# Kernel optimization log

Measured on AMD Instinct MI355X. Metric: run time of the kernel, lower is better.

## Reference

```python
import jax, jax.numpy as jnp
import numpy as np

N, S, C, P, K = 64, 64, 128, 32, 1000   # batch, frames, in_planes, part_num, class_num
HPG = (3 * C) // 16                      # hidden channels per group for part_score mlp = 24
EPS = 1e-5


def setup_inputs() -> dict:
    key = jax.random.key(0)
    ks = jax.random.split(key, 8)
    return {
        "t_f": jax.random.normal(ks[0], (N, S, C, P), jnp.float32),
        "t_s": jax.random.normal(ks[1], (N, S, C, P), jnp.float32),
        "t_l": jax.random.normal(ks[2], (N, S, C, P), jnp.float32),
        # part_score grouped 1x1 convs (groups=P): per-group (out, in)
        "w1": jax.random.normal(ks[3], (P, HPG, 3 * C), jnp.float32) * 0.05,
        "bn1_gamma": jnp.ones((P, HPG), jnp.float32),
        "bn1_beta": jnp.zeros((P, HPG), jnp.float32),
        "w2": jax.random.normal(ks[4], (P, 1, HPG), jnp.float32) * 0.05,
        # decay_channel grouped 1x1 conv: per-group 3C -> C
        "wd": jax.random.normal(ks[5], (P, C, 3 * C), jnp.float32) * 0.05,
        # per-part BatchNorm1d(C) affine params
        "bn_gamma": jnp.ones((P, C), jnp.float32),
        "bn_beta": jnp.zeros((P, C), jnp.float32),
        # fc: (1, C, K) in torch; squeeze leading 1
        "fc": jax.random.normal(ks[6], (C, K), jnp.float32) * 0.05,
    }


def reference(t_f, t_s, t_l, w1, bn1_gamma, bn1_beta, w2, wd, bn_gamma, bn_beta, fc):
    # cat along channel dim then arrange as (n, p, 3c, s) == grouped conv layout
    x = jnp.concatenate([t_f, t_s, t_l], axis=2).transpose(0, 3, 2, 1)  # (n,p,3c,s)

    # --- part_score: grouped 1x1 conv -> BN (batch stats over n,s) -> LeakyReLU -> grouped conv -> sigmoid
    h = jnp.einsum('npis,poi->npos', x, w1)               # (n,p,HPG,s)
    mu = h.mean(axis=(0, 3), keepdims=True)
    var = h.var(axis=(0, 3), keepdims=True)               # biased var (torch training BN)
    h = (h - mu) / jnp.sqrt(var + EPS) * bn1_gamma[None, :, :, None] + bn1_beta[None, :, :, None]
    h = jnp.where(h >= 0, h, 0.01 * h)                    # LeakyReLU(0.01)
    score = jax.nn.sigmoid(jnp.einsum('npis,poi->npos', h, w2))  # (n,p,1,s)

    # --- decay_channel grouped 1x1 conv: 3c -> c per part
    feat = jnp.einsum('npis,poi->npos', x, wd)            # (n,p,c,s)

    # attention-weighted temporal pooling
    wpv = (feat * score).sum(-1) / score.sum(-1)          # (n,p,c)

    # per-part BatchNorm1d over batch dim (training-mode batch stats)
    m = wpv.mean(axis=0)                                  # (p,c)
    v = wpv.var(axis=0)
    part_feature = ((wpv - m) / jnp.sqrt(v + EPS) * bn_gamma + bn_beta).transpose(1, 0, 2)  # (p,n,c)

    part_classification = jnp.einsum('pnc,ck->pnk', part_feature, fc)  # (p,n,K)

    # argmax frame per (n,p) and gather from t_f
    idx = jnp.argmax(score[:, :, 0, :], axis=-1)          # (n,p)
    tfp = t_f.transpose(0, 3, 1, 2)                       # (n,p,s,c)
    selected = jnp.take_along_axis(tfp, idx[:, :, None, None], axis=2)[:, :, 0, :]  # (n,p,c)
    selected_part_feature = selected.transpose(1, 0, 2)   # (p,n,c)

    weighted_part_vector = wpv.transpose(1, 0, 2)         # (p,n,c)
    return part_classification, weighted_part_vector, selected_part_feature
```

## Files before the change

### kernel.cpp

```cpp
#include <hip/hip_runtime.h>
#include <math.h>

#define N 64
#define S 64
#define C 128
#define P 32
#define KCLS 1000
#define HPG 24
#define C3 384
#define NS 4096
#define EPSV 1e-5f

#define WS_H    0
#define WS_W1Z  (WS_H + 2*P*HPG*NS)
#define WS_BNSS (WS_W1Z + 384*8*32*4)
#define WS_Y    (WS_BNSS + P*HPG*2)
#define WS_Z    (WS_Y + P*N*C3)
#define WS_PF   (WS_Z + P*N)
#define WS_SC   (WS_PF + P*C*N)
#define WS_MI   (WS_SC + N*P*S)

__global__ __launch_bounds__(256) void k0w_w1z(
    const float* __restrict__ w1, float* __restrict__ w1z)
{
  int e = blockIdx.x * 256 + threadIdx.x;
  int p = e & 31;
  int r = e >> 5;
  int j = r % 3;
  int r2 = r / 3;
  int og = r2 & 3;
  int i = r2 >> 2;
  float2 v;
  v.x = w1[(p * HPG + og * 6 + j * 2 + 0) * C3 + i];
  v.y = w1[(p * HPG + og * 6 + j * 2 + 1) * C3 + i];
  ((float2*)w1z)[e] = v;
}

__global__ __launch_bounds__(256) void k01_h(
    const float* __restrict__ tf, const float* __restrict__ ts,
    const float* __restrict__ tl, const float* __restrict__ w1z,
    float* __restrict__ h)
{
  int n = blockIdx.x, st = blockIdx.y, split = blockIdx.z;
  int s0 = st * 8;
  int t = threadIdx.x;
  int p = t & 31;
  int og = (t >> 5) & 3;
  int sh = t >> 7;
  __shared__ float xl[8192];
  float acc[6][4];
  #pragma unroll
  for (int oo = 0; oo < 6; ++oo)
    #pragma unroll
    for (int s = 0; s < 4; ++s) acc[oo][s] = 0.f;

  const float2* w2p = (const float2*)w1z;
  const float* srcs[3] = {tf, ts, tl};
  const float* xp = &xl[sh * 4096 + p];

  for (int ch = 0; ch < 6; ++ch) {
    int gch = split * 6 + ch;
    int z = gch >> 2, c0 = (gch & 3) * 32;
    const float* base = srcs[z] + ((size_t)(n * S + s0)) * C * P + c0 * P;
    if (ch) __syncthreads();
    #pragma unroll
    for (int j = 0; j < 8; ++j) {
      int e = t + 256 * j;
      int s_loc = e >> 8;
      int idx = e & 255;
      float4 v = *(const float4*)&base[(size_t)s_loc * C * P + idx * 4];
      *(float4*)&xl[s_loc * 1024 + idx * 4] = v;
    }
    __syncthreads();
    #pragma unroll 4
    for (int cl = 0; cl < 32; ++cl) {
      int i = gch * 32 + cl;
      float xs[4];
      #pragma unroll
      for (int ss = 0; ss < 4; ++ss)
        xs[ss] = xp[ss * 1024 + cl * 32];
      int wb = ((i * 4 + og) * 3) * 32 + p;
      float2 wa  = w2p[wb];
      float2 wbv = w2p[wb + 32];
      float2 wc  = w2p[wb + 64];
      #pragma unroll
      for (int ss = 0; ss < 4; ++ss) {
        acc[0][ss] += wa.x  * xs[ss];
        acc[1][ss] += wa.y  * xs[ss];
        acc[2][ss] += wbv.x * xs[ss];
        acc[3][ss] += wbv.y * xs[ss];
        acc[4][ss] += wc.x  * xs[ss];
        acc[5][ss] += wc.y  * xs[ss];
      }
    }
  }
  #pragma unroll
  for (int oo = 0; oo < 6; ++oo) {
    int o = og * 6 + oo;
    float* hp = h + ((size_t)split * P * HPG + p * HPG + o) * NS + n * S + s0 + sh * 4;
    *(float4*)hp = make_float4(acc[oo][0], acc[oo][1], acc[oo][2], acc[oo][3]);
  }
}

__global__ __launch_bounds__(256) void k2_bnstat(const float* __restrict__ h,
    const float* __restrict__ g, const float* __restrict__ b,
    float* __restrict__ bnss)
{
  int po = blockIdx.x;
  int t = threadIdx.x;
  const float4* r0 = (const float4*)(h + (size_t)po * NS);
  const float4* r1 = (const float4*)(h + (size_t)(P * HPG + po) * NS);
  float sm = 0.f, sq = 0.f;
  #pragma unroll
  for (int k = 0; k < 4; ++k) {
    float4 a = r0[t + 256 * k];
    float4 c = r1[t + 256 * k];
    float v0 = a.x + c.x, v1 = a.y + c.y, v2 = a.z + c.z, v3 = a.w + c.w;
    sm += v0 + v1 + v2 + v3;
    sq += v0 * v0 + v1 * v1 + v2 * v2 + v3 * v3;
  }
  #pragma unroll
  for (int m = 1; m < 64; m <<= 1) {
    sm += __shfl_xor(sm, m, 64);
    sq += __shfl_xor(sq, m, 64);
  }
  __shared__ float red[4][2];
  int w = t >> 6;
  if ((t & 63) == 0) { red[w][0] = sm; red[w][1] = sq; }
  __syncthreads();
  if (t == 0) {
    float sum = red[0][0] + red[1][0] + red[2][0] + red[3][0];
    float ssq = red[0][1] + red[1][1] + red[2][1] + red[3][1];
    float mu  = sum / (float)NS;
    float var = ssq / (float)NS - mu * mu;
    float sc = g[po] * rsqrtf(var + EPSV);
    bnss[po * 2]     = sc;
    bnss[po * 2 + 1] = b[po] - mu * sc;
  }
}

__global__ __launch_bounds__(256) void k3a_score(
    const float* __restrict__ h, const float* __restrict__ bnss,
    const float* __restrict__ w2,
    float* __restrict__ score, float* __restrict__ z,
    int* __restrict__ mi_out)
{
  int n = blockIdx.x;
  int p = blockIdx.y * 4 + (threadIdx.x >> 6);
  int l = threadIdx.x & 63;
  float ssum = 0.f;
  const float* hp0 = h + (size_t)p * HPG * NS + n * S;
  const float* hp1 = hp0 + (size_t)P * HPG * NS;
  #pragma unroll
  for (int o = 0; o < HPG; ++o) {
    float hv = hp0[(size_t)o * NS + l] + hp1[(size_t)o * NS + l];
    float sc = bnss[(p * HPG + o) * 2];
    float sh = bnss[(p * HPG + o) * 2 + 1];
    float v = hv * sc + sh;
    v = (v >= 0.f) ? v : 0.01f * v;
    ssum += w2[p * HPG + o] * v;
  }
  float scr = 1.f / (1.f + expf(-ssum));
  float zs = scr;
  #pragma unroll
  for (int m = 1; m < 64; m <<= 1) zs += __shfl_xor(zs, m, 64);
  float mv = scr; int mi = l;
  #pragma unroll
  for (int m = 1; m < 64; m <<= 1) {
    float ov = __shfl_xor(mv, m, 64);
    int   oi = __shfl_xor(mi, m, 64);
    if (ov > mv || (ov == mv && oi < mi)) { mv = ov; mi = oi; }
  }
  if (l == 0) { z[p * N + n] = zs; mi_out[n * P + p] = mi; }
  score[((size_t)n * P + p) * S + l] = scr;
}

__global__ __launch_bounds__(256) void k3b_y(
    const float* __restrict__ tf, const float* __restrict__ ts,
    const float* __restrict__ tl, const float* __restrict__ score,
    const int* __restrict__ mi, float* __restrict__ y,
    float* __restrict__ out_spf)
{
  int n = blockIdx.x, chunk = blockIdx.y;
  int z = chunk >> 2, c0 = (chunk & 3) * 32;
  const float* src = (z == 0) ? tf : (z == 1) ? ts : tl;
  int t = threadIdx.x;
  int p = t & 31, cl = t >> 5;
  __shared__ float sc_lds[S * P];
  __shared__ int mi_lds[P];
  #pragma unroll
  for (int j = 0; j < 8; ++j) {
    int e = t + 256 * j;
    int s2 = e >> 5, pp = e & 31;
    sc_lds[s2 * P + pp] = score[((size_t)n * P + pp) * S + s2];
  }
  if (t < P) mi_lds[t] = mi[n * P + t];
  __syncthreads();
  int mymi = mi_lds[p];
  const float* base = src + (size_t)n * S * C * P + (size_t)(c0 + cl) * P + p;
  float acc[4] = {0.f, 0.f, 0.f, 0.f};
  float sel[4] = {0.f, 0.f, 0.f, 0.f};
  #pragma unroll 8
  for (int s = 0; s < S; ++s) {
    float scv = sc_lds[s * P + p];
    #pragma unroll
    for (int j = 0; j < 4; ++j) {
      float v = base[(size_t)s * C * P + j * 8 * P];
      acc[j] += v * scv;
      sel[j] = (s == mymi) ? v : sel[j];
    }
  }
  float* yp = y + ((size_t)p * N + n) * C3 + z * C + c0 + cl;
  #pragma unroll
  for (int j = 0; j < 4; ++j) yp[j * 8] = acc[j];
  if (z == 0) {
    float* sp = out_spf + ((size_t)p * N + n) * C + c0 + cl;
    #pragma unroll
    for (int j = 0; j < 4; ++j) sp[j * 8] = sel[j];
  }
}

__global__ __launch_bounds__(256) void k4_wpv(
    const float* __restrict__ y, const float* __restrict__ z,
    const float* __restrict__ wd, const float* __restrict__ g,
    const float* __restrict__ b, float* __restrict__ out_wpv,
    float* __restrict__ pf)
{
  int p   = blockIdx.x;
  int cch = blockIdx.y;
  int t = threadIdx.x;
  int n = t & 63, cg = t >> 6;
  int cbase = cch * 16 + cg * 4;
  __shared__ float ych[96][66];
  float acc[4] = {0.f, 0.f, 0.f, 0.f};
  const float* yp  = y  + (size_t)p * N * C3;
  const float* wdp = wd + (size_t)p * C * C3;
  for (int ch = 0; ch < 4; ++ch) {
    __syncthreads();
    #pragma unroll
    for (int j = 0; j < 24; ++j) {
      int e = t + 256 * j;
      int i = e % 96, nn = e / 96;
      ych[i][nn] = yp[nn * C3 + ch * 96 + i];
    }
    __syncthreads();
    #pragma unroll
    for (int sub = 0; sub < 4; ++sub) {
      float yr[24];
      #pragma unroll
      for (int kk = 0; kk < 24; ++kk) yr[kk] = ych[sub * 24 + kk][n];
      int ibase = ch * 96 + sub * 24;
      #pragma unroll
      for (int cl = 0; cl < 4; ++cl) {
        const float4* w4 = (const float4*)(wdp + (size_t)(cbase + cl) * C3 + ibase);
        float a = 0.f;
        #pragma unroll
        for (int q = 0; q < 6; ++q) {
          float4 wv = w4[q];
          a += yr[q*4+0] * wv.x + yr[q*4+1] * wv.y
             + yr[q*4+2] * wv.z + yr[q*4+3] * wv.w;
        }
        acc[cl] += a;
      }
    }
  }
  float zinv = 1.f / z[p * N + n];
  #pragma unroll
  for (int cl = 0; cl < 4; ++cl) acc[cl] *= zinv;
  #pragma unroll
  for (int cl = 0; cl < 4; ++cl) {
    float v = acc[cl];
    float s = v, q = v * v;
    #pragma unroll
    for (int m = 1; m < 64; m <<= 1) {
      s += __shfl_xor(s, m, 64);
      q += __shfl_xor(q, m, 64);
    }
    float mu  = s * (1.f / 64.f);
    float var = q * (1.f / 64.f) - mu * mu;
    int c = cbase + cl;
    float sc = g[p * C + c] * rsqrtf(var + EPSV);
    float sh = b[p * C + c] - mu * sc;
    pf[((size_t)p * C + c) * N + n] = v * sc + sh;
  }
  float4 wout = make_float4(acc[0], acc[1], acc[2], acc[3]);
  *(float4*)(out_wpv + ((size_t)p * N + n) * C + cbase) = wout;
}

__global__ __launch_bounds__(256) void k5_fc(
    const float* __restrict__ pf, const float* __restrict__ fc,
    float* __restrict__ out0)
{
  int kt = blockIdx.x;
  int p  = blockIdx.y;
  int n0 = blockIdx.z * 16;
  int t = threadIdx.x;
  int k = kt * 256 + t;
  bool ok = k < KCLS;
  int kk = ok ? k : (KCLS - 1);
  float acc[16];
  #pragma unroll
  for (int j = 0; j < 16; ++j) acc[j] = 0.f;
  for (int c = 0; c < C; ++c) {
    float fv = fc[c * KCLS + kk];
    const float4* row4 = (const float4*)(pf + ((size_t)p * C + c) * N + n0);
    #pragma unroll
    for (int j4 = 0; j4 < 4; ++j4) {
      float4 r = row4[j4];
      acc[j4*4+0] += r.x * fv; acc[j4*4+1] += r.y * fv;
      acc[j4*4+2] += r.z * fv; acc[j4*4+3] += r.w * fv;
    }
  }
  if (ok) {
    #pragma unroll 4
    for (int j = 0; j < 16; ++j)
      out0[(size_t)(p * N + n0 + j) * KCLS + k] = acc[j];
  }
}

extern "C" void kernel_launch(void* const* d_in, const int* in_sizes, int n_in,
                              void* d_out, int out_size, void* d_ws, size_t ws_size,
                              hipStream_t stream)
{
  const float* tf = (const float*)d_in[0];
  const float* ts = (const float*)d_in[1];
  const float* tl = (const float*)d_in[2];
  const float* w1 = (const float*)d_in[3];
  const float* g1 = (const float*)d_in[4];
  const float* b1 = (const float*)d_in[5];
  const float* w2 = (const float*)d_in[6];
  const float* wd = (const float*)d_in[7];
  const float* g  = (const float*)d_in[8];
  const float* b  = (const float*)d_in[9];
  const float* fc = (const float*)d_in[10];

  float* ws   = (float*)d_ws;
  float* h    = ws + WS_H;
  float* w1z  = ws + WS_W1Z;
  float* bnss = ws + WS_BNSS;
  float* y    = ws + WS_Y;
  float* z    = ws + WS_Z;
  float* pf   = ws + WS_PF;
  float* sc   = ws + WS_SC;
  int*   mi   = (int*)(ws + WS_MI);

  float* out0 = (float*)d_out;
  float* out1 = out0 + P * N * KCLS;
  float* out2 = out1 + P * N * C;

  k0w_w1z<<<576, 256, 0, stream>>>(w1, w1z);
  k01_h<<<dim3(64, 8, 2), 256, 0, stream>>>(tf, ts, tl, w1z, h);
  k2_bnstat<<<768, 256, 0, stream>>>(h, g1, b1, bnss);
  k3a_score<<<dim3(64, 8), 256, 0, stream>>>(h, bnss, w2, sc, z, mi);
  k3b_y<<<dim3(64, 12), 256, 0, stream>>>(tf, ts, tl, sc, mi, y, out2);
  k4_wpv<<<dim3(32, 8), 256, 0, stream>>>(y, z, wd, g, b, out1, pf);
  k5_fc<<<dim3(4, 32, 4), 256, 0, stream>>>(pf, fc, out0);
}
```

Baseline: 197.1 us.

## Split input-channel reduction across thread halves with 8-frame register tiles in h kernel

```diff
diff --git a/kernel.cpp b/kernel.cpp
--- a/kernel.cpp
+++ b/kernel.cpp
@@ -12,8 +12,8 @@
 #define EPSV 1e-5f
 
 #define WS_H    0
-#define WS_W1Z  (WS_H + 2*P*HPG*NS)
-#define WS_BNSS (WS_W1Z + 384*8*32*4)
+#define WS_W1Z  (WS_H + 4*P*HPG*NS)
+#define WS_BNSS (WS_W1Z + 384*4*3*32*2)
 #define WS_Y    (WS_BNSS + P*HPG*2)
 #define WS_Z    (WS_Y + P*N*C3)
 #define WS_PF   (WS_Z + P*N)
@@ -28,11 +28,11 @@
   int r = e >> 5;
   int j = r % 3;
   int r2 = r / 3;
-  int og = r2 & 3;
+  int oq = r2 & 3;
   int i = r2 >> 2;
   float2 v;
-  v.x = w1[(p * HPG + og * 6 + j * 2 + 0) * C3 + i];
-  v.y = w1[(p * HPG + og * 6 + j * 2 + 1) * C3 + i];
+  v.x = w1[(p * HPG + oq * 6 + j * 2 + 0) * C3 + i];
+  v.y = w1[(p * HPG + oq * 6 + j * 2 + 1) * C3 + i];
   ((float2*)w1z)[e] = v;
 }
 
@@ -45,46 +45,51 @@
   int s0 = st * 8;
   int t = threadIdx.x;
   int p = t & 31;
-  int og = (t >> 5) & 3;
-  int sh = t >> 7;
+  int oq = (t >> 5) & 3;
+  int ih = t >> 7;
   __shared__ float xl[8192];
-  float acc[6][4];
+  float acc[6][8];
   #pragma unroll
   for (int oo = 0; oo < 6; ++oo)
     #pragma unroll
-    for (int s = 0; s < 4; ++s) acc[oo][s] = 0.f;
+    for (int s = 0; s < 8; ++s) acc[oo][s] = 0.f;
 
   const float2* w2p = (const float2*)w1z;
   const float* srcs[3] = {tf, ts, tl};
-  const float* xp = &xl[sh * 4096 + p];
 
   for (int ch = 0; ch < 6; ++ch) {
     int gch = split * 6 + ch;
     int z = gch >> 2, c0 = (gch & 3) * 32;
-    const float* base = srcs[z] + ((size_t)(n * S + s0)) * C * P + c0 * P;
+    const float* tb = srcs[z] + ((size_t)(n * S + s0)) * C * P + c0 * P;
     if (ch) __syncthreads();
     #pragma unroll
     for (int j = 0; j < 8; ++j) {
-      int e = t + 256 * j;
-      int s_loc = e >> 8;
-      int idx = e & 255;
-      float4 v = *(const float4*)&base[(size_t)s_loc * C * P + idx * 4];
-      *(float4*)&xl[s_loc * 1024 + idx * 4] = v;
+      int a = (t + 256 * j) * 4;
+      int c  = a >> 8;
+      int sh = (a >> 7) & 1;
+      int pp = (a >> 2) & 31;
+      const float* g = tb + (size_t)(sh * 4) * C * P + c * P + pp;
+      float4 v;
+      v.x = g[0];
+      v.y = g[(size_t)1 * C * P];
+      v.z = g[(size_t)2 * C * P];
+      v.w = g[(size_t)3 * C * P];
+      *(float4*)&xl[a] = v;
     }
     __syncthreads();
     #pragma unroll 4
-    for (int cl = 0; cl < 32; ++cl) {
+    for (int k = 0; k < 16; ++k) {
+      int cl = ih * 16 + k;
       int i = gch * 32 + cl;
-      float xs[4];
-      #pragma unroll
-      for (int ss = 0; ss < 4; ++ss)
-        xs[ss] = xp[ss * 1024 + cl * 32];
-      int wb = ((i * 4 + og) * 3) * 32 + p;
+      int wb = ((i * 4 + oq) * 3) * 32 + p;
       float2 wa  = w2p[wb];
       float2 wbv = w2p[wb + 32];
       float2 wc  = w2p[wb + 64];
+      float4 x0 = *(const float4*)&xl[cl * 256 + p * 4];
+      float4 x1 = *(const float4*)&xl[cl * 256 + 128 + p * 4];
+      float xs[8] = {x0.x, x0.y, x0.z, x0.w, x1.x, x1.y, x1.z, x1.w};
       #pragma unroll
-      for (int ss = 0; ss < 4; ++ss) {
+      for (int ss = 0; ss < 8; ++ss) {
         acc[0][ss] += wa.x  * xs[ss];
         acc[1][ss] += wa.y  * xs[ss];
         acc[2][ss] += wbv.x * xs[ss];
@@ -94,11 +99,13 @@
       }
     }
   }
+  int q = split * 2 + ih;
   #pragma unroll
   for (int oo = 0; oo < 6; ++oo) {
-    int o = og * 6 + oo;
-    float* hp = h + ((size_t)split * P * HPG + p * HPG + o) * NS + n * S + s0 + sh * 4;
-    *(float4*)hp = make_float4(acc[oo][0], acc[oo][1], acc[oo][2], acc[oo][3]);
+    int o = oq * 6 + oo;
+    float* hp = h + ((size_t)q * P * HPG + p * HPG + o) * NS + n * S + s0;
+    *(float4*)&hp[0] = make_float4(acc[oo][0], acc[oo][1], acc[oo][2], acc[oo][3]);
+    *(float4*)&hp[4] = make_float4(acc[oo][4], acc[oo][5], acc[oo][6], acc[oo][7]);
   }
 }
 
@@ -110,12 +117,21 @@
   int t = threadIdx.x;
   const float4* r0 = (const float4*)(h + (size_t)po * NS);
   const float4* r1 = (const float4*)(h + (size_t)(P * HPG + po) * NS);
+  const float4* r2 = (const float4*)(h + (size_t)(2 * P * HPG + po) * NS);
+  const float4* r3 = (const float4*)(h + (size_t)(3 * P * HPG + po) * NS);
   float sm = 0.f, sq = 0.f;
   #pragma unroll
   for (int k = 0; k < 4; ++k) {
     float4 a = r0[t + 256 * k];
     float4 c = r1[t + 256 * k];
-    float v0 = a.x + c.x, v1 = a.y + c.y, v2 = a.z + c.z, v3 = a.w + c.w;
+    float d = 0.f;
+    float4 e4 = r2[t + 256 * k];
+    float4 f4 = r3[t + 256 * k];
+    float v0 = a.x + c.x + e4.x + f4.x;
+    float v1 = a.y + c.y + e4.y + f4.y;
+    float v2 = a.z + c.z + e4.z + f4.z;
+    float v3 = a.w + c.w + e4.w + f4.w;
+    (void)d;
     sm += v0 + v1 + v2 + v3;
     sq += v0 * v0 + v1 * v1 + v2 * v2 + v3 * v3;
   }
@@ -151,9 +167,12 @@
   float ssum = 0.f;
   const float* hp0 = h + (size_t)p * HPG * NS + n * S;
   const float* hp1 = hp0 + (size_t)P * HPG * NS;
+  const float* hp2 = hp0 + (size_t)2 * P * HPG * NS;
+  const float* hp3 = hp0 + (size_t)3 * P * HPG * NS;
   #pragma unroll
   for (int o = 0; o < HPG; ++o) {
-    float hv = hp0[(size_t)o * NS + l] + hp1[(size_t)o * NS + l];
+    float hv = hp0[(size_t)o * NS + l] + hp1[(size_t)o * NS + l]
+             + hp2[(size_t)o * NS + l] + hp3[(size_t)o * NS + l];
     float sc = bnss[(p * HPG + o) * 2];
     float sh = bnss[(p * HPG + o) * 2 + 1];
     float v = hv * sc + sh;
```

Result: faster. 185.0 us (-6.1%).
